# Kernel optimization log

Hardware: AMD Instinct MI355X
Metric: run time of the kernel (lower is better)

Reference implementation:

```python
import jax, jax.numpy as jnp
import numpy as np

IN_FEATURES = 8192
OUT_FEATURES = 512
SPARSITY_FACTOR = IN_FEATURES // OUT_FEATURES  # 16


def _band_mask(out_features, in_features, sf, dtype):
    # mask[i, j] = 1 iff j in [i*sf, (i+1)*sf)
    rows = jnp.arange(out_features)[:, None]          # [O,1]
    cols = jnp.arange(in_features)[None, :] // sf     # [1,I]
    return (cols == rows).astype(dtype)               # [O,I]


def setup_inputs() -> dict:
    key = jax.random.key(0)
    k1, k2, k3 = jax.random.split(key, 3)
    x = jax.random.normal(k1, (4096, IN_FEATURES), dtype=jnp.float32)
    weight = jax.random.normal(k2, (OUT_FEATURES, IN_FEATURES), dtype=jnp.float32)
    bias = jax.random.normal(k3, (OUT_FEATURES,), dtype=jnp.float32)
    return {"x": x, "weight": weight, "bias": bias}


def reference(x, weight, bias):
    out_f, in_f = weight.shape
    sf = in_f // out_f
    mask = _band_mask(out_f, in_f, sf, weight.dtype)
    masked_weight = mask * weight                     # [O,I]
    # F.linear: x @ masked_weight.T + bias
    return jnp.einsum('bi,oi->bo', x, masked_weight) + bias
```

## Files before the change

### kernel.cpp

```cpp
#include <hip/hip_runtime.h>
#include <hip/hip_bf16.h>

#define IN_FEATURES  8192
#define OUT_FEATURES 512
#define SF           16
#define BATCH        4096

__global__ __launch_bounds__(256) void banded_linear_kernel(
    const float* __restrict__ x,
    const float* __restrict__ w,
    const float* __restrict__ bias,
    float* __restrict__ out)
{
    const int tid = blockIdx.x * blockDim.x + threadIdx.x;
    const int o = tid & (OUT_FEATURES - 1);
    const int b = tid >> 9;

    const float4* __restrict__ xp =
        reinterpret_cast<const float4*>(x + ((size_t)b << 13) + ((size_t)o << 4));
    const float4* __restrict__ wp =
        reinterpret_cast<const float4*>(w + (size_t)o * (IN_FEATURES + SF));

    float acc = 0.0f;
#pragma unroll
    for (int k = 0; k < 4; ++k) {
        const float4 xv = xp[k];
        const float4 wv = wp[k];
        acc = fmaf(xv.x, wv.x, acc);
        acc = fmaf(xv.y, wv.y, acc);
        acc = fmaf(xv.z, wv.z, acc);
        acc = fmaf(xv.w, wv.w, acc);
    }
    out[tid] = acc + bias[o];
}

extern "C" void kernel_launch(void* const* d_in, const int* in_sizes, int n_in,
                              void* d_out, int out_size, void* d_ws, size_t ws_size,
                              hipStream_t stream) {
    const float* x    = (const float*)d_in[0];
    const float* w    = (const float*)d_in[1];
    const float* bias = (const float*)d_in[2];
    float* out = (float*)d_out;

    const int total = BATCH * OUT_FEATURES;
    const int block = 256;
    const int grid  = total / block;
    banded_linear_kernel<<<grid, block, 0, stream>>>(x, w, bias, out);
}
```

Measured before the change: 29.60 us.

## Split each band dot across 4 lanes with shuffles and loop over batch rows

Four lanes now share each output's 16-element dot product. Each lane loads one float4, so adjacent lanes read contiguous x memory, and a two-step xor-shuffle reduces the partial sums. Each thread keeps its weight and bias in registers and loops over 16 batch rows, which removes repeated weight loads. In exchange it adds shuffle overhead, only one lane in four writes output (a strided store pattern), and the grid launches fewer threads.

After: 25.36 us. 14.3% less time.

```diff
diff --git a/kernel.cpp b/kernel.cpp
--- a/kernel.cpp
+++ b/kernel.cpp
@@ -5,6 +5,7 @@
 #define OUT_FEATURES 512
 #define SF           16
 #define BATCH        4096
+#define B_ITERS      16
 
 __global__ __launch_bounds__(256) void banded_linear_kernel(
     const float* __restrict__ x,
@@ -12,26 +13,30 @@
     const float* __restrict__ bias,
     float* __restrict__ out)
 {
-    const int tid = blockIdx.x * blockDim.x + threadIdx.x;
-    const int o = tid & (OUT_FEATURES - 1);
-    const int b = tid >> 9;
+    const int gid  = blockIdx.x * blockDim.x + threadIdx.x;
+    const int j    = gid & 3;
+    const int o    = (gid >> 2) & (OUT_FEATURES - 1);
+    const int slab = gid >> 11;
 
-    const float4* __restrict__ xp =
-        reinterpret_cast<const float4*>(x + ((size_t)b << 13) + ((size_t)o << 4));
-    const float4* __restrict__ wp =
-        reinterpret_cast<const float4*>(w + (size_t)o * (IN_FEATURES + SF));
+    const float4 wv = *reinterpret_cast<const float4*>(
+        w + (size_t)o * (IN_FEATURES + SF) + (j << 2));
+    const float bv = bias[o];
 
-    float acc = 0.0f;
-#pragma unroll
-    for (int k = 0; k < 4; ++k) {
-        const float4 xv = xp[k];
-        const float4 wv = wp[k];
-        acc = fmaf(xv.x, wv.x, acc);
-        acc = fmaf(xv.y, wv.y, acc);
-        acc = fmaf(xv.z, wv.z, acc);
-        acc = fmaf(xv.w, wv.w, acc);
+    const float* xbase = x + ((size_t)slab * B_ITERS << 13) + ((size_t)o << 4) + (j << 2);
+    float* obase = out + ((size_t)slab * B_ITERS << 9) + o;
+
+#pragma unroll 4
+    for (int i = 0; i < B_ITERS; ++i) {
+        const float4 xv = *reinterpret_cast<const float4*>(xbase + ((size_t)i << 13));
+        float acc = fmaf(xv.x, wv.x,
+                    fmaf(xv.y, wv.y,
+                    fmaf(xv.z, wv.z, xv.w * wv.w)));
+        acc += __shfl_xor(acc, 1, 64);
+        acc += __shfl_xor(acc, 2, 64);
+        if (j == 0) {
+            obase[(size_t)i << 9] = acc + bv;
+        }
     }
-    out[tid] = acc + bias[o];
 }
 
 extern "C" void kernel_launch(void* const* d_in, const int* in_sizes, int n_in,
@@ -42,8 +47,7 @@
     const float* bias = (const float*)d_in[2];
     float* out = (float*)d_out;
 
-    const int total = BATCH * OUT_FEATURES;
     const int block = 256;
-    const int grid  = total / block;
+    const int grid  = (BATCH / B_ITERS) * OUT_FEATURES * 4 / block;
     banded_linear_kernel<<<grid, block, 0, stream>>>(x, w, bias, out);
 }
```
